# Optimization experiments

Hardware: AMD Instinct MI355X
Metric: run time of the kernel (lower is better)

The kernel has to match this reference:

```python
import jax, jax.numpy as jnp
import numpy as np

B = 32
N_INPUTS = 16384
N_DET = 65536
K = 32  # max_inputs_per_detector


def setup_inputs() -> dict:
    key = jax.random.key(0)
    k1, k2 = jax.random.split(key)
    x = jax.random.normal(k1, (B, N_INPUTS), dtype=jnp.float32)
    # detector membership table: each detector watches K input neuron ids
    detectors = jax.random.randint(k2, (N_DET, K), 0, N_INPUTS, dtype=jnp.int32)
    return {"x": x, "detectors": detectors}


def reference(x, detectors):
    """Winner-take-all inhibition.

    For each batch row and each detector, the member input with the largest
    activation is the winner; every other (valid, id != -1) member is
    inhibited (its winning_stat is incremented). Output spikes (1.0) only for
    inputs never inhibited by any detector (winning_stat == 0), matching
    spiking_inhibition=True where the output is a pure binary mask.
    """
    Bn, n_inputs = x.shape
    D, Kd = detectors.shape
    valid = detectors >= 0                      # [D, K] (-1 = padding)
    safe_idx = jnp.where(valid, detectors, 0)   # [D, K]
    neg_inf = jnp.float32(-jnp.inf)
    col = jnp.arange(Kd, dtype=jnp.int32)[None, :]

    def per_batch(xb):  # xb: [n_inputs]
        vals = jnp.where(valid, xb[safe_idx], neg_inf)     # [D, K] gather
        widx = jnp.argmax(vals, axis=-1)                   # winner slot per detector
        loser = valid & (col != widx[:, None])             # inhibited members
        stat = jnp.zeros((n_inputs,), jnp.int32).at[safe_idx.reshape(-1)].add(
            loser.reshape(-1).astype(jnp.int32))           # scatter-add counts
        return stat

    stat = jax.vmap(per_batch)(x)               # [B, n_inputs]
    out = (stat == 0).astype(jnp.float32)       # spike iff never inhibited
    return out
```

## Files before the change

### kernel.cpp

```cpp
#include <hip/hip_runtime.h>

#define N_INPUTS 16384
#define N_DET    65536
#define KD       32
#define BATCH    32
#define SLICES   16
#define DPB      (N_DET / SLICES)
#define THREADS  1024

__device__ __forceinline__ float max3f(float a, float b, float c) {
    return fmaxf(fmaxf(a, b), c);
}

__device__ __forceinline__ unsigned compact_even(unsigned v) {
    v &= 0x55555555u;
    v = (v | (v >> 1)) & 0x33333333u;
    v = (v | (v >> 2)) & 0x0F0F0F0Fu;
    v = (v | (v >> 4)) & 0x00FF00FFu;
    v = (v | (v >> 8)) & 0x0000FFFFu;
    return v;
}

__global__ __launch_bounds__(THREADS) void inhibit(const float* __restrict__ x,
                                                   const int* __restrict__ det,
                                                   unsigned long long* __restrict__ pm) {
    __shared__ float2   xs[N_INPUTS];
    __shared__ unsigned fl[N_INPUTS / 16];

    const int slice = blockIdx.x;
    const int pair  = blockIdx.y;
    const int tid   = threadIdx.x;

    fl[tid] = 0u;

    const float4* x0 = (const float4*)(x + (size_t)(2 * pair) * N_INPUTS);
    const float4* x1 = (const float4*)(x + (size_t)(2 * pair + 1) * N_INPUTS);
    float4* xs4 = (float4*)xs;
#pragma unroll
    for (int k = 0; k < N_INPUTS / 4 / THREADS; ++k) {
        int t = tid + k * THREADS;
        float4 a = x0[t], b = x1[t];
        xs4[2 * t + 0] = make_float4(a.x, b.x, a.y, b.y);
        xs4[2 * t + 1] = make_float4(a.z, b.z, a.w, b.w);
    }
    __syncthreads();

    const int4* det4 = (const int4*)det;
#pragma unroll 1
    for (int j = 0; j < DPB / THREADS; ++j) {
        const int   d    = slice * DPB + j * THREADS + tid;
        const int4* drow = det4 + (size_t)d * 8;
        int ids[KD];
#pragma unroll
        for (int q = 0; q < 8; ++q) {
            int4 r = drow[q];
            ids[q * 4 + 0] = r.x; ids[q * 4 + 1] = r.y;
            ids[q * 4 + 2] = r.z; ids[q * 4 + 3] = r.w;
        }

        float2 v[KD];
#pragma unroll
        for (int s = 0; s < KD; ++s) v[s] = xs[ids[s]];

        float t0[11], t1[11];
#pragma unroll
        for (int i = 0; i < 10; ++i) {
            t0[i] = max3f(v[3 * i].x, v[3 * i + 1].x, v[3 * i + 2].x);
            t1[i] = max3f(v[3 * i].y, v[3 * i + 1].y, v[3 * i + 2].y);
        }
        t0[10] = fmaxf(v[30].x, v[31].x);
        t1[10] = fmaxf(v[30].y, v[31].y);
        float m0 = fmaxf(max3f(max3f(t0[0], t0[1], t0[2]),
                               max3f(t0[3], t0[4], t0[5]),
                               max3f(t0[6], t0[7], t0[8])),
                         fmaxf(t0[9], t0[10]));
        float m1 = fmaxf(max3f(max3f(t1[0], t1[1], t1[2]),
                               max3f(t1[3], t1[4], t1[5]),
                               max3f(t1[6], t1[7], t1[8])),
                         fmaxf(t1[9], t1[10]));

        int s0 = 0, s1 = 0;
#pragma unroll
        for (int s = KD - 1; s >= 0; --s) {
            s0 = (v[s].x == m0) ? s : s0;
            s1 = (v[s].y == m1) ? s : s1;
        }

        const unsigned wm0 = 1u << s0, wm1 = 1u << s1;
#pragma unroll
        for (int s = 0; s < KD; ++s) {
            int id = ids[s];
            unsigned lose = 3u ^ (((wm0 >> s) & 1u) | (((wm1 >> s) & 1u) << 1));
            atomicOr(&fl[id >> 4], lose << ((id & 15) * 2));
        }
    }
    __syncthreads();

    unsigned f  = fl[tid];
    unsigned b0 = compact_even(f);
    unsigned b1 = compact_even(f >> 1);
    unsigned short* pm0 =
        (unsigned short*)(pm + ((size_t)(2 * pair) * SLICES + slice) * (N_INPUTS / 64));
    unsigned short* pm1 =
        (unsigned short*)(pm + ((size_t)(2 * pair + 1) * SLICES + slice) * (N_INPUTS / 64));
    pm0[tid] = (unsigned short)b0;
    pm1[tid] = (unsigned short)b1;
}

__global__ __launch_bounds__(256) void finalize(const unsigned* __restrict__ pm,
                                                float* __restrict__ out) {
    const int gid = blockIdx.x * 256 + threadIdx.x;
    const int b   = gid >> 14;
    const int i   = gid & (N_INPUTS - 1);
    unsigned acc = 0;
#pragma unroll
    for (int s = 0; s < SLICES; ++s)
        acc |= pm[((b * SLICES + s) << 9) + (i >> 5)];
    out[gid] = ((acc >> (i & 31)) & 1u) ? 0.0f : 1.0f;
}

extern "C" void kernel_launch(void* const* d_in, const int* in_sizes, int n_in,
                              void* d_out, int out_size, void* d_ws, size_t ws_size,
                              hipStream_t stream) {
    const float* x   = (const float*)d_in[0];
    const int*   det = (const int*)d_in[1];
    unsigned long long* pm = (unsigned long long*)d_ws;

    dim3 grid(SLICES, BATCH / 2);
    inhibit<<<grid, THREADS, 0, stream>>>(x, det, pm);
    finalize<<<BATCH * N_INPUTS / 256, 256, 0, stream>>>((const unsigned*)pm,
                                                         (float*)d_out);
}
```

Measured before the change: 85.41 us.

## Replace per-member loser atomics with winner counts compared against input degree

Instead of OR-ing a loser bit for all 32 members of each detector, the inhibit kernel now atomically increments only a per-input win counter for the winner, and a separate kernel counts how many detectors each input belongs to. An input spikes iff its win count equals its degree. This cuts shared-memory atomics in the hot loop from 32 to 2 per detector, at the cost of an extra degree-count kernel and larger workspace traffic. The 8-bit packed counters can overflow if an input's degree reaches 256, which assumes small per-input degrees; the degree counts are recomputed on every call, so the extra kernel's work is part of the timed time.

New measurement: 98.80 us. +15.7%, slower.

```diff
diff --git a/kernel.cpp b/kernel.cpp
--- a/kernel.cpp
+++ b/kernel.cpp
@@ -5,33 +5,58 @@
 #define KD       32
 #define BATCH    32
 #define SLICES   16
+#define PAIRS    (BATCH / 2)
 #define DPB      (N_DET / SLICES)
 #define THREADS  1024
+
+#define DEG_BLOCKS     64
+#define DET_PER_DEGBLK (N_DET / DEG_BLOCKS)
+#define DEG_WORDS      (N_INPUTS / 4)
+#define WC_WORDS       (N_INPUTS / 2)
 
 __device__ __forceinline__ float max3f(float a, float b, float c) {
     return fmaxf(fmaxf(a, b), c);
 }
 
-__device__ __forceinline__ unsigned compact_even(unsigned v) {
-    v &= 0x55555555u;
-    v = (v | (v >> 1)) & 0x33333333u;
-    v = (v | (v >> 2)) & 0x0F0F0F0Fu;
-    v = (v | (v >> 4)) & 0x00FF00FFu;
-    v = (v | (v >> 8)) & 0x0000FFFFu;
-    return v;
+
+__global__ __launch_bounds__(1024) void degree_count(const int* __restrict__ det,
+                                                     unsigned* __restrict__ degp) {
+    __shared__ unsigned dl[DEG_WORDS];
+    const int tid = threadIdx.x;
+#pragma unroll
+    for (int k = 0; k < DEG_WORDS / 1024; ++k) dl[tid + k * 1024] = 0u;
+    __syncthreads();
+
+    const int d = blockIdx.x * DET_PER_DEGBLK + tid;
+    const int4* drow = (const int4*)det + (size_t)d * (KD / 4);
+#pragma unroll
+    for (int q = 0; q < KD / 4; ++q) {
+        int4 r = drow[q];
+        atomicAdd(&dl[r.x >> 2], 1u << (8 * (r.x & 3)));
+        atomicAdd(&dl[r.y >> 2], 1u << (8 * (r.y & 3)));
+        atomicAdd(&dl[r.z >> 2], 1u << (8 * (r.z & 3)));
+        atomicAdd(&dl[r.w >> 2], 1u << (8 * (r.w & 3)));
+    }
+    __syncthreads();
+
+    unsigned* out = degp + (size_t)blockIdx.x * DEG_WORDS;
+#pragma unroll
+    for (int k = 0; k < DEG_WORDS / 1024; ++k)
+        out[tid + k * 1024] = dl[tid + k * 1024];
 }
 
 __global__ __launch_bounds__(THREADS) void inhibit(const float* __restrict__ x,
                                                    const int* __restrict__ det,
-                                                   unsigned long long* __restrict__ pm) {
+                                                   unsigned* __restrict__ wp) {
     __shared__ float2   xs[N_INPUTS];
-    __shared__ unsigned fl[N_INPUTS / 16];
+    __shared__ unsigned wc[WC_WORDS];
 
     const int slice = blockIdx.x;
     const int pair  = blockIdx.y;
     const int tid   = threadIdx.x;
 
-    fl[tid] = 0u;
+#pragma unroll
+    for (int k = 0; k < WC_WORDS / THREADS; ++k) wc[tid + k * THREADS] = 0u;
 
     const float4* x0 = (const float4*)(x + (size_t)(2 * pair) * N_INPUTS);
     const float4* x1 = (const float4*)(x + (size_t)(2 * pair + 1) * N_INPUTS);
@@ -79,44 +104,60 @@
                                max3f(t1[6], t1[7], t1[8])),
                          fmaxf(t1[9], t1[10]));
 
-        int s0 = 0, s1 = 0;
+        int i0 = ids[0], i1 = ids[0];
 #pragma unroll
         for (int s = KD - 1; s >= 0; --s) {
-            s0 = (v[s].x == m0) ? s : s0;
-            s1 = (v[s].y == m1) ? s : s1;
+            i0 = (v[s].x == m0) ? ids[s] : i0;
+            i1 = (v[s].y == m1) ? ids[s] : i1;
         }
 
-        const unsigned wm0 = 1u << s0, wm1 = 1u << s1;
-#pragma unroll
-        for (int s = 0; s < KD; ++s) {
-            int id = ids[s];
-            unsigned lose = 3u ^ (((wm0 >> s) & 1u) | (((wm1 >> s) & 1u) << 1));
-            atomicOr(&fl[id >> 4], lose << ((id & 15) * 2));
-        }
+        atomicAdd(&wc[i0 >> 1], 1u << (8 * ((i0 & 1) * 2 + 0)));
+        atomicAdd(&wc[i1 >> 1], 1u << (8 * ((i1 & 1) * 2 + 1)));
     }
     __syncthreads();
 
-    unsigned f  = fl[tid];
-    unsigned b0 = compact_even(f);
-    unsigned b1 = compact_even(f >> 1);
-    unsigned short* pm0 =
-        (unsigned short*)(pm + ((size_t)(2 * pair) * SLICES + slice) * (N_INPUTS / 64));
-    unsigned short* pm1 =
-        (unsigned short*)(pm + ((size_t)(2 * pair + 1) * SLICES + slice) * (N_INPUTS / 64));
-    pm0[tid] = (unsigned short)b0;
-    pm1[tid] = (unsigned short)b1;
+    unsigned* out = wp + (size_t)(slice * PAIRS + pair) * WC_WORDS;
+#pragma unroll
+    for (int k = 0; k < WC_WORDS / THREADS; ++k)
+        out[tid + k * THREADS] = wc[tid + k * THREADS];
 }
 
-__global__ __launch_bounds__(256) void finalize(const unsigned* __restrict__ pm,
-                                                float* __restrict__ out) {
-    const int gid = blockIdx.x * 256 + threadIdx.x;
-    const int b   = gid >> 14;
-    const int i   = gid & (N_INPUTS - 1);
-    unsigned acc = 0;
+__global__ __launch_bounds__(1024) void finalize(const unsigned* __restrict__ wp,
+                                                 const unsigned* __restrict__ degp,
+                                                 float* __restrict__ out) {
+    __shared__ unsigned red[1024];
+    const int k = blockIdx.x, t = threadIdx.x;
+
+    red[t] = degp[(size_t)(t >> 4) * DEG_WORDS + k * 16 + (t & 15)];
+    __syncthreads();
+#pragma unroll
+    for (int off = 512; off >= 16; off >>= 1) {
+        if (t < off) red[t] += red[t + off];
+        __syncthreads();
+    }
+
+    const int b  = t & 31;
+    const int jp = t >> 5;
+    const int p  = b >> 1, q = b & 1;
+
+    unsigned wsum = 0;
 #pragma unroll
     for (int s = 0; s < SLICES; ++s)
-        acc |= pm[((b * SLICES + s) << 9) + (i >> 5)];
-    out[gid] = ((acc >> (i & 31)) & 1u) ? 0.0f : 1.0f;
+        wsum += wp[(size_t)(s * PAIRS + p) * WC_WORDS + k * 32 + jp];
+
+    const unsigned w0 = (wsum >> (8 * q)) & 255u;
+    const unsigned w1 = (wsum >> (8 * (2 + q))) & 255u;
+
+    const unsigned dw = red[jp >> 1];
+    const int      sh = (2 * jp) & 3;
+    const unsigned d0 = (dw >> (8 * sh)) & 255u;
+    const unsigned d1 = (dw >> (8 * (sh + 1))) & 255u;
+
+    float2 r;
+    r.x = (w0 == d0) ? 1.0f : 0.0f;
+    r.y = (w1 == d1) ? 1.0f : 0.0f;
+    const size_t i0 = (size_t)k * 64 + 2 * jp;
+    *(float2*)(out + (size_t)b * N_INPUTS + i0) = r;
 }
 
 extern "C" void kernel_launch(void* const* d_in, const int* in_sizes, int n_in,
@@ -124,10 +165,11 @@
                               hipStream_t stream) {
     const float* x   = (const float*)d_in[0];
     const int*   det = (const int*)d_in[1];
-    unsigned long long* pm = (unsigned long long*)d_ws;
+    unsigned* wp   = (unsigned*)d_ws;
+    unsigned* degp = (unsigned*)d_ws + (size_t)SLICES * PAIRS * WC_WORDS;
 
-    dim3 grid(SLICES, BATCH / 2);
-    inhibit<<<grid, THREADS, 0, stream>>>(x, det, pm);
-    finalize<<<BATCH * N_INPUTS / 256, 256, 0, stream>>>((const unsigned*)pm,
-                                                         (float*)d_out);
+    degree_count<<<DEG_BLOCKS, 1024, 0, stream>>>(det, degp);
+    dim3 grid(SLICES, PAIRS);
+    inhibit<<<grid, THREADS, 0, stream>>>(x, det, wp);
+    finalize<<<N_INPUTS / 64, 1024, 0, stream>>>(wp, degp, (float*)d_out);
 }
```

## Prefetch all detector ids and software-pipeline LDS gathers across detector iterations

Applied to the files above, without the earlier changes.

Loads all four detector rows' ids into registers up front, so the global loads issue together rather than serially per iteration. The gather/compute loop is unrolled into a double-buffered schedule where the next detector's LDS gathers are issued before the current detector's max/argmax/atomic work. Launch bounds now declare one block per CU, letting the compiler use more registers for the 128 ids and two 32-entry float2 buffers. The risk is high VGPR pressure and possible spills. Occupancy was already limited to one 1024-thread block by the 130KB of shared memory.

Measured after the change: 193.3 us. 126% more time.

```diff
diff --git a/kernel.cpp b/kernel.cpp
--- a/kernel.cpp
+++ b/kernel.cpp
@@ -21,9 +21,9 @@
     return v;
 }
 
-__global__ __launch_bounds__(THREADS) void inhibit(const float* __restrict__ x,
-                                                   const int* __restrict__ det,
-                                                   unsigned long long* __restrict__ pm) {
+__global__ __launch_bounds__(THREADS, 1) void inhibit(const float* __restrict__ x,
+                                                      const int* __restrict__ det,
+                                                      unsigned long long* __restrict__ pm) {
     __shared__ float2   xs[N_INPUTS];
     __shared__ unsigned fl[N_INPUTS / 16];
 
@@ -46,54 +46,66 @@
     __syncthreads();
 
     const int4* det4 = (const int4*)det;
-#pragma unroll 1
-    for (int j = 0; j < DPB / THREADS; ++j) {
-        const int   d    = slice * DPB + j * THREADS + tid;
-        const int4* drow = det4 + (size_t)d * 8;
-        int ids[KD];
+    int ids[4][KD];
+#pragma unroll
+    for (int j = 0; j < 4; ++j) {
+        const int4* drow = det4 + (size_t)(slice * DPB + j * THREADS + tid) * 8;
 #pragma unroll
         for (int q = 0; q < 8; ++q) {
             int4 r = drow[q];
-            ids[q * 4 + 0] = r.x; ids[q * 4 + 1] = r.y;
-            ids[q * 4 + 2] = r.z; ids[q * 4 + 3] = r.w;
-        }
-
-        float2 v[KD];
-#pragma unroll
-        for (int s = 0; s < KD; ++s) v[s] = xs[ids[s]];
-
-        float t0[11], t1[11];
-#pragma unroll
-        for (int i = 0; i < 10; ++i) {
-            t0[i] = max3f(v[3 * i].x, v[3 * i + 1].x, v[3 * i + 2].x);
-            t1[i] = max3f(v[3 * i].y, v[3 * i + 1].y, v[3 * i + 2].y);
-        }
-        t0[10] = fmaxf(v[30].x, v[31].x);
-        t1[10] = fmaxf(v[30].y, v[31].y);
-        float m0 = fmaxf(max3f(max3f(t0[0], t0[1], t0[2]),
-                               max3f(t0[3], t0[4], t0[5]),
-                               max3f(t0[6], t0[7], t0[8])),
-                         fmaxf(t0[9], t0[10]));
-        float m1 = fmaxf(max3f(max3f(t1[0], t1[1], t1[2]),
-                               max3f(t1[3], t1[4], t1[5]),
-                               max3f(t1[6], t1[7], t1[8])),
-                         fmaxf(t1[9], t1[10]));
-
-        int s0 = 0, s1 = 0;
-#pragma unroll
-        for (int s = KD - 1; s >= 0; --s) {
-            s0 = (v[s].x == m0) ? s : s0;
-            s1 = (v[s].y == m1) ? s : s1;
-        }
-
-        const unsigned wm0 = 1u << s0, wm1 = 1u << s1;
-#pragma unroll
-        for (int s = 0; s < KD; ++s) {
-            int id = ids[s];
-            unsigned lose = 3u ^ (((wm0 >> s) & 1u) | (((wm1 >> s) & 1u) << 1));
-            atomicOr(&fl[id >> 4], lose << ((id & 15) * 2));
+            ids[j][4 * q + 0] = r.x; ids[j][4 * q + 1] = r.y;
+            ids[j][4 * q + 2] = r.z; ids[j][4 * q + 3] = r.w;
         }
     }
+
+    float2 vA[KD], vB[KD];
+
+#define GATHER(vbuf, J)                                                        \
+    _Pragma("unroll") for (int s = 0; s < KD; ++s) vbuf[s] = xs[ids[J][s]];
+
+#define COMPUTE(v, J)                                                          \
+    {                                                                          \
+        float t0[11], t1[11];                                                  \
+        _Pragma("unroll") for (int i = 0; i < 10; ++i) {                       \
+            t0[i] = max3f(v[3 * i].x, v[3 * i + 1].x, v[3 * i + 2].x);         \
+            t1[i] = max3f(v[3 * i].y, v[3 * i + 1].y, v[3 * i + 2].y);         \
+        }                                                                      \
+        t0[10] = fmaxf(v[30].x, v[31].x);                                      \
+        t1[10] = fmaxf(v[30].y, v[31].y);                                      \
+        float m0 = fmaxf(max3f(max3f(t0[0], t0[1], t0[2]),                     \
+                               max3f(t0[3], t0[4], t0[5]),                     \
+                               max3f(t0[6], t0[7], t0[8])),                    \
+                         fmaxf(t0[9], t0[10]));                                \
+        float m1 = fmaxf(max3f(max3f(t1[0], t1[1], t1[2]),                     \
+                               max3f(t1[3], t1[4], t1[5]),                     \
+                               max3f(t1[6], t1[7], t1[8])),                    \
+                         fmaxf(t1[9], t1[10]));                                \
+        int s0 = 0, s1 = 0;                                                    \
+        _Pragma("unroll") for (int s = KD - 1; s >= 0; --s) {                  \
+            s0 = (v[s].x == m0) ? s : s0;                                      \
+            s1 = (v[s].y == m1) ? s : s1;                                      \
+        }                                                                      \
+        const unsigned wm0 = 1u << s0, wm1 = 1u << s1;                         \
+        _Pragma("unroll") for (int s = 0; s < KD; ++s) {                       \
+            int id = ids[J][s];                                                \
+            unsigned lose =                                                    \
+                3u ^ (((wm0 >> s) & 1u) | (((wm1 >> s) & 1u) << 1));           \
+            atomicOr(&fl[id >> 4], lose << ((id & 15) * 2));                   \
+        }                                                                      \
+    }
+
+    GATHER(vA, 0)
+    GATHER(vB, 1)
+    COMPUTE(vA, 0)
+    GATHER(vA, 2)
+    COMPUTE(vB, 1)
+    GATHER(vB, 3)
+    COMPUTE(vA, 2)
+    COMPUTE(vB, 3)
+
+#undef GATHER
+#undef COMPUTE
+
     __syncthreads();
 
     unsigned f  = fl[tid];
```

## Use 16-bit order-preserving keys for four batches per block with exact-tie repair

Applied to the files above, without the earlier changes.

Adds a prep kernel that turns x into 16-bit monotonic keys packed four batch rows per 64-bit word. Each inhibit block then gathers one word per member and handles four batches with packed u16 max and 4-bit loser flags. Because truncating to 16 bits can create ties, any detector with more than one member matching the max key is queued. A repair kernel rescans those from the full float values and marks the extra losers. Slices, threads per block and occupancy change, and finalize writes float4 vectors, at the cost of two more launches, a memset and a global atomic queue whose length depends on the data.

After: 269.9 us. 3.16x slower.

```diff
diff --git a/kernel.cpp b/kernel.cpp
--- a/kernel.cpp
+++ b/kernel.cpp
@@ -4,48 +4,66 @@
 #define N_DET    65536
 #define KD       32
 #define BATCH    32
-#define SLICES   16
+#define SLICES   32
+#define QUADS    8
 #define DPB      (N_DET / SLICES)
-#define THREADS  1024
-
-__device__ __forceinline__ float max3f(float a, float b, float c) {
-    return fmaxf(fmaxf(a, b), c);
-}
-
-__device__ __forceinline__ unsigned compact_even(unsigned v) {
-    v &= 0x55555555u;
-    v = (v | (v >> 1)) & 0x33333333u;
-    v = (v | (v >> 2)) & 0x0F0F0F0Fu;
-    v = (v | (v >> 4)) & 0x00FF00FFu;
-    v = (v | (v >> 8)) & 0x0000FFFFu;
+#define THREADS  512
+
+typedef unsigned short u16x4 __attribute__((ext_vector_type(4)));
+
+__device__ __forceinline__ unsigned short key16(float f) {
+    unsigned b = __float_as_uint(f);
+    unsigned m = ((unsigned)((int)b >> 31)) | 0x80000000u;
+    return (unsigned short)((b ^ m) >> 16);
+}
+
+__device__ __forceinline__ unsigned c8(unsigned v, int q) {
+    v = (v >> q) & 0x11111111u;
+    v = (v | (v >> 3)) & 0x03030303u;
+    v = (v | (v >> 6)) & 0x000F000Fu;
+    v = (v | (v >> 12)) & 0xFFu;
     return v;
 }
 
-__global__ __launch_bounds__(THREADS) void inhibit(const float* __restrict__ x,
-                                                   const int* __restrict__ det,
-                                                   unsigned long long* __restrict__ pm) {
-    __shared__ float2   xs[N_INPUTS];
-    __shared__ unsigned fl[N_INPUTS / 16];
+__global__ __launch_bounds__(1024) void prep(const float* __restrict__ x,
+                                             unsigned long long* __restrict__ xq) {
+    const int gid  = blockIdx.x * 1024 + threadIdx.x;
+    const int quad = gid >> 14, i = gid & (N_INPUTS - 1);
+    const float* xb = x + (size_t)quad * 4 * N_INPUTS + i;
+    unsigned long long k = 0;
+#pragma unroll
+    for (int q = 0; q < 4; ++q)
+        k |= (unsigned long long)key16(xb[(size_t)q * N_INPUTS]) << (16 * q);
+    xq[gid] = k;
+}
+
+__global__ __launch_bounds__(THREADS, 2) void inhibit(
+        const unsigned long long* __restrict__ xq,
+        const int* __restrict__ det,
+        unsigned* __restrict__ pm,
+        unsigned* __restrict__ qcnt,
+        unsigned* __restrict__ queue) {
+    __shared__ __align__(16) unsigned long long xs[N_INPUTS];
+    __shared__ unsigned fl[N_INPUTS / 8];
 
     const int slice = blockIdx.x;
-    const int pair  = blockIdx.y;
+    const int quad  = blockIdx.y;
     const int tid   = threadIdx.x;
 
-    fl[tid] = 0u;
-
-    const float4* x0 = (const float4*)(x + (size_t)(2 * pair) * N_INPUTS);
-    const float4* x1 = (const float4*)(x + (size_t)(2 * pair + 1) * N_INPUTS);
-    float4* xs4 = (float4*)xs;
-#pragma unroll
-    for (int k = 0; k < N_INPUTS / 4 / THREADS; ++k) {
-        int t = tid + k * THREADS;
-        float4 a = x0[t], b = x1[t];
-        xs4[2 * t + 0] = make_float4(a.x, b.x, a.y, b.y);
-        xs4[2 * t + 1] = make_float4(a.z, b.z, a.w, b.w);
-    }
+#pragma unroll
+    for (int k = 0; k < (N_INPUTS / 8) / THREADS; ++k)
+        fl[tid + k * THREADS] = 0u;
+
+    const ulonglong2* src = (const ulonglong2*)(xq + (size_t)quad * N_INPUTS);
+    ulonglong2* dst = (ulonglong2*)xs;
+#pragma unroll
+    for (int k = 0; k < N_INPUTS / 2 / THREADS; ++k)
+        dst[tid + k * THREADS] = src[tid + k * THREADS];
     __syncthreads();
 
     const int4* det4 = (const int4*)det;
+    const u16x4* xsv = (const u16x4*)xs;
+
 #pragma unroll 1
     for (int j = 0; j < DPB / THREADS; ++j) {
         const int   d    = slice * DPB + j * THREADS + tid;
@@ -58,65 +76,108 @@
             ids[q * 4 + 2] = r.z; ids[q * 4 + 3] = r.w;
         }
 
-        float2 v[KD];
-#pragma unroll
-        for (int s = 0; s < KD; ++s) v[s] = xs[ids[s]];
-
-        float t0[11], t1[11];
-#pragma unroll
-        for (int i = 0; i < 10; ++i) {
-            t0[i] = max3f(v[3 * i].x, v[3 * i + 1].x, v[3 * i + 2].x);
-            t1[i] = max3f(v[3 * i].y, v[3 * i + 1].y, v[3 * i + 2].y);
-        }
-        t0[10] = fmaxf(v[30].x, v[31].x);
-        t1[10] = fmaxf(v[30].y, v[31].y);
-        float m0 = fmaxf(max3f(max3f(t0[0], t0[1], t0[2]),
-                               max3f(t0[3], t0[4], t0[5]),
-                               max3f(t0[6], t0[7], t0[8])),
-                         fmaxf(t0[9], t0[10]));
-        float m1 = fmaxf(max3f(max3f(t1[0], t1[1], t1[2]),
-                               max3f(t1[3], t1[4], t1[5]),
-                               max3f(t1[6], t1[7], t1[8])),
-                         fmaxf(t1[9], t1[10]));
-
-        int s0 = 0, s1 = 0;
-#pragma unroll
-        for (int s = KD - 1; s >= 0; --s) {
-            s0 = (v[s].x == m0) ? s : s0;
-            s1 = (v[s].y == m1) ? s : s1;
-        }
-
-        const unsigned wm0 = 1u << s0, wm1 = 1u << s1;
+        u16x4 k[KD];
+#pragma unroll
+        for (int s = 0; s < KD; ++s) k[s] = xsv[ids[s]];
+
+        u16x4 t[16];
+#pragma unroll
+        for (int i = 0; i < 16; ++i) t[i] = __builtin_elementwise_max(k[2 * i], k[2 * i + 1]);
+#pragma unroll
+        for (int i = 0; i < 8; ++i)  t[i] = __builtin_elementwise_max(t[2 * i], t[2 * i + 1]);
+#pragma unroll
+        for (int i = 0; i < 4; ++i)  t[i] = __builtin_elementwise_max(t[2 * i], t[2 * i + 1]);
+        t[0] = __builtin_elementwise_max(t[0], t[1]);
+        t[2] = __builtin_elementwise_max(t[2], t[3]);
+        const u16x4 km = __builtin_elementwise_max(t[0], t[2]);
+
+        unsigned eq0 = 0, eq1 = 0, eq2 = 0, eq3 = 0;
 #pragma unroll
         for (int s = 0; s < KD; ++s) {
+            eq0 |= (unsigned)(k[s][0] == km[0]) << s;
+            eq1 |= (unsigned)(k[s][1] == km[1]) << s;
+            eq2 |= (unsigned)(k[s][2] == km[2]) << s;
+            eq3 |= (unsigned)(k[s][3] == km[3]) << s;
+        }
+
+#pragma unroll
+        for (int s = 0; s < KD; ++s) {
+            unsigned nib = 0xFu ^ (((eq0 >> s) & 1u) | (((eq1 >> s) & 1u) << 1) |
+                                  (((eq2 >> s) & 1u) << 2) | (((eq3 >> s) & 1u) << 3));
             int id = ids[s];
-            unsigned lose = 3u ^ (((wm0 >> s) & 1u) | (((wm1 >> s) & 1u) << 1));
-            atomicOr(&fl[id >> 4], lose << ((id & 15) * 2));
+            atomicOr(&fl[id >> 3], nib << ((id & 7) * 4));
+        }
+
+#pragma unroll
+        for (int q = 0; q < 4; ++q) {
+            unsigned eqq = (q == 0) ? eq0 : (q == 1) ? eq1 : (q == 2) ? eq2 : eq3;
+            if (__builtin_popcount(eqq) > 1) {
+                unsigned pos = atomicAdd(qcnt, 1u);
+                queue[2 * pos]     = (unsigned)d | ((unsigned)(quad * 4 + q) << 16);
+                queue[2 * pos + 1] = eqq;
+            }
         }
     }
     __syncthreads();
 
-    unsigned f  = fl[tid];
-    unsigned b0 = compact_even(f);
-    unsigned b1 = compact_even(f >> 1);
-    unsigned short* pm0 =
-        (unsigned short*)(pm + ((size_t)(2 * pair) * SLICES + slice) * (N_INPUTS / 64));
-    unsigned short* pm1 =
-        (unsigned short*)(pm + ((size_t)(2 * pair + 1) * SLICES + slice) * (N_INPUTS / 64));
-    pm0[tid] = (unsigned short)b0;
-    pm1[tid] = (unsigned short)b1;
+#pragma unroll 1
+    for (int q = 0; q < 4; ++q) {
+        unsigned w0 = fl[4 * tid + 0], w1 = fl[4 * tid + 1];
+        unsigned w2 = fl[4 * tid + 2], w3 = fl[4 * tid + 3];
+        unsigned out32 = c8(w0, q) | (c8(w1, q) << 8) | (c8(w2, q) << 16) | (c8(w3, q) << 24);
+        pm[((size_t)(slice * BATCH + quad * 4 + q)) * (N_INPUTS / 32) + tid] = out32;
+    }
+}
+
+__global__ __launch_bounds__(256) void repair(const int* __restrict__ det,
+                                              const float* __restrict__ x,
+                                              const unsigned* __restrict__ queue,
+                                              const unsigned* __restrict__ qcnt,
+                                              unsigned* __restrict__ pm) {
+    const unsigned total = *qcnt;
+    for (unsigned idx = blockIdx.x * 256 + threadIdx.x; idx < total;
+         idx += gridDim.x * 256) {
+        const unsigned rec = queue[2 * idx];
+        const unsigned eq  = queue[2 * idx + 1];
+        const int d = rec & 0xFFFFu, b = rec >> 16;
+        const int* drow = det + (size_t)d * KD;
+        const float* xb = x + (size_t)b * N_INPUTS;
+
+        float best = -__builtin_inff(); int bs = 0;
+        unsigned m = eq;
+        while (m) {
+            int s = __builtin_ctz(m); m &= m - 1;
+            float v = xb[drow[s]];
+            if (v > best) { best = v; bs = s; }
+        }
+        m = eq & ~(1u << bs);
+        const unsigned base = (unsigned)((d >> 11) * BATCH + b) * (N_INPUTS / 32);
+        while (m) {
+            int s = __builtin_ctz(m); m &= m - 1;
+            int id = drow[s];
+            atomicOr(&pm[base + (id >> 5)], 1u << (id & 31));
+        }
+    }
 }
 
 __global__ __launch_bounds__(256) void finalize(const unsigned* __restrict__ pm,
                                                 float* __restrict__ out) {
-    const int gid = blockIdx.x * 256 + threadIdx.x;
-    const int b   = gid >> 14;
-    const int i   = gid & (N_INPUTS - 1);
+    const int t = blockIdx.x * 256 + threadIdx.x;
+    const int b = t >> 9, g = t & 511;
     unsigned acc = 0;
 #pragma unroll
     for (int s = 0; s < SLICES; ++s)
-        acc |= pm[((b * SLICES + s) << 9) + (i >> 5)];
-    out[gid] = ((acc >> (i & 31)) & 1u) ? 0.0f : 1.0f;
+        acc |= pm[((size_t)(s * BATCH + b)) * (N_INPUTS / 32) + g];
+    float4* o = (float4*)(out + (size_t)b * N_INPUTS + g * 32);
+#pragma unroll
+    for (int v = 0; v < 8; ++v) {
+        float4 r;
+        r.x = ((acc >> (4 * v + 0)) & 1u) ? 0.0f : 1.0f;
+        r.y = ((acc >> (4 * v + 1)) & 1u) ? 0.0f : 1.0f;
+        r.z = ((acc >> (4 * v + 2)) & 1u) ? 0.0f : 1.0f;
+        r.w = ((acc >> (4 * v + 3)) & 1u) ? 0.0f : 1.0f;
+        o[v] = r;
+    }
 }
 
 extern "C" void kernel_launch(void* const* d_in, const int* in_sizes, int n_in,
@@ -124,10 +185,17 @@
                               hipStream_t stream) {
     const float* x   = (const float*)d_in[0];
     const int*   det = (const int*)d_in[1];
-    unsigned long long* pm = (unsigned long long*)d_ws;
-
-    dim3 grid(SLICES, BATCH / 2);
-    inhibit<<<grid, THREADS, 0, stream>>>(x, det, pm);
-    finalize<<<BATCH * N_INPUTS / 256, 256, 0, stream>>>((const unsigned*)pm,
-                                                         (float*)d_out);
-}
+
+    unsigned* pm   = (unsigned*)d_ws;
+    unsigned* qcnt = (unsigned*)((char*)d_ws + (2u << 20));
+    unsigned* queue = (unsigned*)((char*)d_ws + (2u << 20) + 4096);
+    unsigned long long* xq =
+        (unsigned long long*)((char*)d_ws + (18u << 20) + 4096);
+
+    prep<<<QUADS * N_INPUTS / 1024, 1024, 0, stream>>>(x, xq);
+    hipMemsetAsync(qcnt, 0, 4, stream);
+    dim3 grid(SLICES, QUADS);
+    inhibit<<<grid, THREADS, 0, stream>>>(xq, det, pm, qcnt, queue);
+    repair<<<64, 256, 0, stream>>>(det, x, queue, qcnt, pm);
+    finalize<<<BATCH * (N_INPUTS / 32) / 256, 256, 0, stream>>>(pm, (float*)d_out);
+}
```
